# Kernel tuning notes

Measured on AMD Instinct MI355X. Metric: run time of the kernel, lower is better.

Reference implementation:

```python
import jax, jax.numpy as jnp
import numpy as np

NUM_BASES = 5
STRIDE = (1, 1)
PADDING = ((1, 1), (1, 1))
DN = ('NCHW', 'OIHW', 'NCHW')


def quantize_act(x):
    # Q_A_DOREFA forward: round(clamp(x, 0, 1)) -> values in {0, 1}
    return jnp.round(jnp.clip(x, 0.0, 1.0))


def quantize_w(w):
    # Q_W forward: sign(w) * mean(|w|) over the whole weight tensor of one basis
    return jnp.sign(w) * jnp.mean(jnp.abs(w))


def setup_inputs() -> dict:
    key = jax.random.key(0)
    kx, kw = jax.random.split(key)
    x = jax.random.normal(kx, (8, 256, 64, 64), dtype=jnp.float32)
    # 5 bases, each an OIHW conv kernel [256, 256, 3, 3]
    weights = jax.random.normal(kw, (NUM_BASES, 256, 256, 3, 3), dtype=jnp.float32) * 0.05
    return {"x": x, "weights": weights}


def reference(x, weights):
    xq = quantize_act(x)
    # quantize each basis independently (per-basis scalar scale)
    wq = jax.vmap(quantize_w)(weights)  # [5, O, I, kh, kw]
    # conv is linear in the kernel: sum of 5 convs == conv with summed kernels
    w_sum = jnp.sum(wq, axis=0)
    out = jax.lax.conv_general_dilated(
        xq, w_sum, window_strides=STRIDE, padding=PADDING,
        dimension_numbers=DN)
    return out / NUM_BASES
```

## Files before the change

kernel.cpp:

```cpp
#include <hip/hip_runtime.h>
#include <hip/hip_bf16.h>

typedef __attribute__((ext_vector_type(4))) int i32x4;

constexpr int NB = 8, CI = 256, OC = 256, HH = 64, WW = 64, HP = 66, WP = 66;
constexpr int NBASES = 5;
constexpr int WELEMS = OC * CI * 9;
constexpr int NT = 36;

__global__ void k_abs_partial(const float* __restrict__ w, float* __restrict__ part) {
    int b = blockIdx.x >> 6, chunk = blockIdx.x & 63;
    const float4* v = (const float4*)(w + (size_t)b * WELEMS + (size_t)chunk * (WELEMS / 64));
    float s = 0.f;
    for (int i = threadIdx.x; i < WELEMS / 64 / 4; i += 256) {
        float4 t = v[i];
        s += fabsf(t.x) + fabsf(t.y) + fabsf(t.z) + fabsf(t.w);
    }
    #pragma unroll
    for (int off = 32; off; off >>= 1) s += __shfl_down(s, off, 64);
    __shared__ float ls[4];
    int lane = threadIdx.x & 63, wid = threadIdx.x >> 6;
    if (lane == 0) ls[wid] = s;
    __syncthreads();
    if (threadIdx.x == 0) part[blockIdx.x] = ls[0] + ls[1] + ls[2] + ls[3];
}

__global__ void k_prep(const float* __restrict__ w, const float* __restrict__ part,
                       signed char* __restrict__ wsum8, float* __restrict__ scl,
                       const float* __restrict__ x, signed char* __restrict__ xq) {
    __shared__ float sLDS[NBASES];
    int tid = threadIdx.x;

    if (blockIdx.x < OC) {
        if (tid < 64) {
            #pragma unroll
            for (int b = 0; b < NBASES; ++b) {
                float v = part[b * 64 + tid];
                #pragma unroll
                for (int off = 32; off; off >>= 1) v += __shfl_down(v, off, 64);
                if (tid == 0) sLDS[b] = v * (1.0f / (float)WELEMS);
            }
        }
        __syncthreads();
        float sc[NBASES];
        #pragma unroll
        for (int b = 0; b < NBASES; ++b) sc[b] = sLDS[b];
        float sSum = sc[0] + sc[1] + sc[2] + sc[3] + sc[4];
        float invS = 127.0f / sSum;
        if (blockIdx.x == 0 && tid == 0)
            scl[0] = sSum * (0.2f / 127.0f);

        int o = blockIdx.x, i = tid;
        const float* base = w + ((size_t)(o * CI + i)) * 9;
        float acc[9];
        #pragma unroll
        for (int t = 0; t < 9; ++t) acc[t] = 0.f;
        #pragma unroll
        for (int b = 0; b < NBASES; ++b) {
            const float* wb = base + (size_t)b * WELEMS;
            #pragma unroll
            for (int t = 0; t < 9; ++t) {
                float xv = wb[t];
                acc[t] += (xv > 0.f) ? sc[b] : ((xv < 0.f) ? -sc[b] : 0.f);
            }
        }
        #pragma unroll
        for (int t = 0; t < 9; ++t)
            wsum8[(t * OC + o) * CI + i] = (signed char)__float2int_rn(acc[t] * invS);
        return;
    }

    int nh = blockIdx.x - OC, n = nh >> 6, h = nh & 63;
    const float* xb = x + ((size_t)n * CI) * (HH * WW) + h * WW;
    signed char* ob = xq + ((size_t)(n * HP + (h + 1)) * WP + 1) * CI;
    int w4 = tid >> 2;
    int cl = tid & 3;
    #pragma unroll
    for (int p = 0; p < 4; ++p) {
        int c = (p * 4 + cl) * 16;
        signed char pk[16];
        #pragma unroll
        for (int i = 0; i < 16; ++i) {
            float v = xb[(size_t)(c + i) * (HH * WW) + w4];
            pk[i] = (signed char)rintf(fminf(fmaxf(v, 0.f), 1.f));
        }
        *(int4*)(ob + w4 * CI + c) = *(const int4*)pk;
    }
    (ob - CI)[tid] = 0;
    (ob + 64 * CI)[tid] = 0;
    if (h == 0) {
        signed char* r0 = xq + ((size_t)(n * HP + 0) * WP) * CI;
        int4 z = {0, 0, 0, 0};
        for (int i = tid; i < WP * CI / 16; i += 256) *(int4*)(r0 + i * 16) = z;
    }
    if (h == HH - 1) {
        signed char* r65 = xq + ((size_t)(n * HP + (HP - 1)) * WP) * CI;
        int4 z = {0, 0, 0, 0};
        for (int i = tid; i < WP * CI / 16; i += 256) *(int4*)(r65 + i * 16) = z;
    }
}

__launch_bounds__(256, 2)
__global__ void k_conv(const signed char* __restrict__ xq,
                       const signed char* __restrict__ wsum,
                       const float* __restrict__ scl,
                       float* __restrict__ out) {
    __shared__ __align__(16) signed char lA[3][128 * 64];
    __shared__ __align__(16) signed char lB[3][128 * 64];

    float so = scl[0];

    int bid = blockIdx.x;
    int bx = ((bid & 7) << 6) | (bid >> 3);
    int pt = bx >> 1, ot = bx & 1;
    int pb = pt * 128;
    int n = pb >> 12;
    int h0 = (pb >> 6) & 63;
    int oc0 = ot * 128;
    int tid = threadIdx.x;

    int base0 = (n * HP + h0) * WP * CI;
    int bBase0 = oc0 * CI;

    int aOff[2], bOff[2];
    #pragma unroll
    for (int k = 0; k < 2; ++k) {
        int c = tid + k * 256;
        int row = c >> 2, sp = c & 3;
        int l = sp ^ ((row >> 1) & 3);
        aOff[k] = ((row >> 6) * WP + (row & 63)) * CI + l * 16;
        bOff[k] = row * CI + l * 16;
    }

    int lane = tid & 63, wid = tid >> 6;
    int wm = wid >> 1, wn = wid & 1;
    int g = lane >> 4, r16 = lane & 15;
    int fA[4], fB[4];
    #pragma unroll
    for (int q = 0; q < 4; ++q) {
        int ra = wm * 64 + q * 16 + r16;
        fA[q] = ra * 64 + (g ^ ((ra >> 1) & 3)) * 16;
        int rb = wn * 64 + q * 16 + r16;
        fB[q] = rb * 64 + (g ^ ((rb >> 1) & 3)) * 16;
    }

    i32x4 acc[4][4] = {};

    auto stage = [&](int t) {
        int buf = t % 3;
        int tap = t >> 2;
        int c0 = (t & 3) << 6;
        int kh = (tap * 171) >> 9;
        int kw = tap - kh * 3;
        const signed char* aSrc = xq + base0 + (kh * WP + kw) * CI + c0;
        const signed char* bSrc = wsum + tap * (OC * CI) + bBase0 + c0;
        #pragma unroll
        for (int k = 0; k < 2; ++k) {
            __builtin_amdgcn_global_load_lds(
                (const __attribute__((address_space(1))) void*)(aSrc + aOff[k]),
                (__attribute__((address_space(3))) void*)(&lA[buf][(tid + k * 256) * 16]), 16, 0, 0);
            __builtin_amdgcn_global_load_lds(
                (const __attribute__((address_space(1))) void*)(bSrc + bOff[k]),
                (__attribute__((address_space(3))) void*)(&lB[buf][(tid + k * 256) * 16]), 16, 0, 0);
        }
    };

    stage(0); stage(1);

    #pragma unroll 1
    for (int t = 0; t < NT; ++t) {
        int buf = t % 3;
        if (t < NT - 1) asm volatile("s_waitcnt vmcnt(4)" ::: "memory");
        else            asm volatile("s_waitcnt vmcnt(0)" ::: "memory");
        __builtin_amdgcn_s_barrier();
        if (t + 2 < NT) stage(t + 2);

        i32x4 aR[4], bR[4];
        #pragma unroll
        for (int q = 0; q < 4; ++q) aR[q] = *(const i32x4*)&lA[buf][fA[q]];
        #pragma unroll
        for (int q = 0; q < 4; ++q) bR[q] = *(const i32x4*)&lB[buf][fB[q]];
        asm volatile("s_waitcnt lgkmcnt(0)" ::: "memory");
        __builtin_amdgcn_sched_barrier(0);
        __builtin_amdgcn_s_setprio(1);
        #pragma unroll
        for (int mq = 0; mq < 4; ++mq)
            #pragma unroll
            for (int nq = 0; nq < 4; ++nq)
                acc[mq][nq] = __builtin_amdgcn_mfma_i32_16x16x64_i8(
                    aR[mq], bR[nq], acc[mq][nq], 0, 0, 0);
        __builtin_amdgcn_s_setprio(0);
    }

    int hw0 = pb & 4095;
    #pragma unroll
    for (int mq = 0; mq < 4; ++mq) {
        int pl = wm * 64 + mq * 16 + g * 4;
        #pragma unroll
        for (int nq = 0; nq < 4; ++nq) {
            int oc = oc0 + wn * 64 + nq * 16 + r16;
            float4 v;
            v.x = (float)acc[mq][nq][0] * so;
            v.y = (float)acc[mq][nq][1] * so;
            v.z = (float)acc[mq][nq][2] * so;
            v.w = (float)acc[mq][nq][3] * so;
            *(float4*)(out + ((size_t)(n * OC + oc) << 12) + hw0 + pl) = v;
        }
    }
}

extern "C" void kernel_launch(void* const* d_in, const int* in_sizes, int n_in,
                              void* d_out, int out_size, void* d_ws, size_t ws_size,
                              hipStream_t stream) {
    (void)in_sizes; (void)n_in; (void)out_size; (void)ws_size;
    const float* x   = (const float*)d_in[0];
    const float* wts = (const float*)d_in[1];
    float* out = (float*)d_out;
    char* wsb = (char*)d_ws;
    float* part          = (float*)wsb;
    float* scl           = (float*)(wsb + 2048);
    signed char* wsum8   = (signed char*)(wsb + 4096);
    signed char* xq8     = (signed char*)(wsb + (size_t)(2u << 20));

    hipLaunchKernelGGL(k_abs_partial, dim3(NBASES * 64), dim3(256), 0, stream, wts, part);
    hipLaunchKernelGGL(k_prep, dim3(OC + NB * HH), dim3(256), 0, stream,
                       wts, part, wsum8, scl, x, xq8);
    hipLaunchKernelGGL(k_conv, dim3((NB * HH * WW / 128) * (OC / 128)), dim3(256), 0, stream,
                       xq8, wsum8, scl, out);
}
```

Baseline: 53.68 us.

## Give each wave private LDS staging to drop per-step workgroup barriers

Each wave now loads its own A and B slices (its 64 pixels and 64 output channels) into a private double-buffered LDS region, so the per-iteration workgroup barrier is removed. The aim is to stop waves stalling on each other at every k-step. The cost is that A and B are no longer shared across waves: each tile is fetched twice from global memory (8 loads per stage instead of 4). The layout also drops the XOR swizzle, which may add LDS bank conflicts, and the buffer depth goes from triple to double.

```diff
diff --git a/kernel.cpp b/kernel.cpp
--- a/kernel.cpp
+++ b/kernel.cpp
@@ -105,10 +105,7 @@
                        const signed char* __restrict__ wsum,
                        const float* __restrict__ scl,
                        float* __restrict__ out) {
-    __shared__ __align__(16) signed char lA[3][128 * 64];
-    __shared__ __align__(16) signed char lB[3][128 * 64];
-
-    float so = scl[0];
+    __shared__ __align__(16) signed char lds[4][2][8192];
 
     int bid = blockIdx.x;
     int bx = ((bid & 7) << 6) | (bid >> 3);
@@ -120,68 +117,53 @@
     int tid = threadIdx.x;
 
     int base0 = (n * HP + h0) * WP * CI;
-    int bBase0 = oc0 * CI;
-
-    int aOff[2], bOff[2];
-    #pragma unroll
-    for (int k = 0; k < 2; ++k) {
-        int c = tid + k * 256;
-        int row = c >> 2, sp = c & 3;
-        int l = sp ^ ((row >> 1) & 3);
-        aOff[k] = ((row >> 6) * WP + (row & 63)) * CI + l * 16;
-        bOff[k] = row * CI + l * 16;
-    }
 
     int lane = tid & 63, wid = tid >> 6;
     int wm = wid >> 1, wn = wid & 1;
     int g = lane >> 4, r16 = lane & 15;
-    int fA[4], fB[4];
-    #pragma unroll
-    for (int q = 0; q < 4; ++q) {
-        int ra = wm * 64 + q * 16 + r16;
-        fA[q] = ra * 64 + (g ^ ((ra >> 1) & 3)) * 16;
-        int rb = wn * 64 + q * 16 + r16;
-        fB[q] = rb * 64 + (g ^ ((rb >> 1) & 3)) * 16;
-    }
+
+    int aSrcLane = (wm * WP + lane) * CI;
+    int bSrcLane = (oc0 + wn * 64 + lane) * CI;
+    int fOff[4];
+    #pragma unroll
+    for (int q = 0; q < 4; ++q) fOff[q] = g * 1024 + (q * 16 + r16) * 16;
 
     i32x4 acc[4][4] = {};
 
     auto stage = [&](int t) {
-        int buf = t % 3;
+        int buf = t & 1;
         int tap = t >> 2;
         int c0 = (t & 3) << 6;
         int kh = (tap * 171) >> 9;
         int kw = tap - kh * 3;
-        const signed char* aSrc = xq + base0 + (kh * WP + kw) * CI + c0;
-        const signed char* bSrc = wsum + tap * (OC * CI) + bBase0 + c0;
-        #pragma unroll
-        for (int k = 0; k < 2; ++k) {
+        const signed char* aS = xq + base0 + (kh * WP + kw) * CI + c0 + aSrcLane;
+        const signed char* bS = wsum + tap * (OC * CI) + c0 + bSrcLane;
+        #pragma unroll
+        for (int s = 0; s < 4; ++s)
             __builtin_amdgcn_global_load_lds(
-                (const __attribute__((address_space(1))) void*)(aSrc + aOff[k]),
-                (__attribute__((address_space(3))) void*)(&lA[buf][(tid + k * 256) * 16]), 16, 0, 0);
+                (const __attribute__((address_space(1))) void*)(aS + s * 16),
+                (__attribute__((address_space(3))) void*)(&lds[wid][buf][s * 1024 + lane * 16]),
+                16, 0, 0);
+        #pragma unroll
+        for (int s = 0; s < 4; ++s)
             __builtin_amdgcn_global_load_lds(
-                (const __attribute__((address_space(1))) void*)(bSrc + bOff[k]),
-                (__attribute__((address_space(3))) void*)(&lB[buf][(tid + k * 256) * 16]), 16, 0, 0);
-        }
+                (const __attribute__((address_space(1))) void*)(bS + s * 16),
+                (__attribute__((address_space(3))) void*)(&lds[wid][buf][4096 + s * 1024 + lane * 16]),
+                16, 0, 0);
     };
 
     stage(0); stage(1);
 
     #pragma unroll 1
     for (int t = 0; t < NT; ++t) {
-        int buf = t % 3;
-        if (t < NT - 1) asm volatile("s_waitcnt vmcnt(4)" ::: "memory");
+        if (t < NT - 1) asm volatile("s_waitcnt vmcnt(8)" ::: "memory");
         else            asm volatile("s_waitcnt vmcnt(0)" ::: "memory");
-        __builtin_amdgcn_s_barrier();
-        if (t + 2 < NT) stage(t + 2);
-
+        const signed char* B = &lds[wid][t & 1][0];
         i32x4 aR[4], bR[4];
         #pragma unroll
-        for (int q = 0; q < 4; ++q) aR[q] = *(const i32x4*)&lA[buf][fA[q]];
-        #pragma unroll
-        for (int q = 0; q < 4; ++q) bR[q] = *(const i32x4*)&lB[buf][fB[q]];
-        asm volatile("s_waitcnt lgkmcnt(0)" ::: "memory");
-        __builtin_amdgcn_sched_barrier(0);
+        for (int q = 0; q < 4; ++q) aR[q] = *(const i32x4*)(B + fOff[q]);
+        #pragma unroll
+        for (int q = 0; q < 4; ++q) bR[q] = *(const i32x4*)(B + 4096 + fOff[q]);
         __builtin_amdgcn_s_setprio(1);
         #pragma unroll
         for (int mq = 0; mq < 4; ++mq)
@@ -190,8 +172,13 @@
                 acc[mq][nq] = __builtin_amdgcn_mfma_i32_16x16x64_i8(
                     aR[mq], bR[nq], acc[mq][nq], 0, 0, 0);
         __builtin_amdgcn_s_setprio(0);
-    }
-
+        if (t + 2 < NT) {
+            asm volatile("s_waitcnt lgkmcnt(0)" ::: "memory");
+            stage(t + 2);
+        }
+    }
+
+    float so = scl[0];
     int hw0 = pb & 4095;
     #pragma unroll
     for (int mq = 0; mq < 4; ++mq) {
```

Result: slower. 97.00 us (+80.7%).
